# Performance work log

Measured on AMD Instinct MI355X. Metric: run time of the kernel, lower is better.

Reference implementation:

```python
import jax, jax.numpy as jnp
import numpy as np

B, T, D, S = 16, 16384, 256, 4
EPS = 1e-12  # matches torch F.normalize eps


def setup_inputs() -> dict:
    key = jax.random.key(0)
    k1, k2 = jax.random.split(key)
    embeddings = jax.random.normal(k1, (B, T, D), dtype=jnp.float32)
    spk = jax.random.randint(k2, (B, T), 0, S)
    labels = jax.nn.one_hot(spk, S, dtype=jnp.float32)  # [B,T,S] one-hot speaker indicators
    return {"embeddings": embeddings, "labels": labels}


def reference(embeddings, labels):
    # embeddings: [B,T,D], labels: [B,T,S]
    Bv, Tv, _ = embeddings.shape
    # row-wise L2 normalize (torch F.normalize semantics: v / max(||v||, eps))
    n = jnp.linalg.norm(embeddings, axis=-1, keepdims=True)
    V = embeddings / jnp.maximum(n, EPS)
    Y = labels
    # ||V V^T - Y Y^T||_F^2 = ||V^T V||_F^2 - 2||V^T Y||_F^2 + ||Y^T Y||_F^2
    Gvv = jnp.einsum('btd,bte->bde', V, V)   # [B,D,D]
    Gvy = jnp.einsum('btd,bts->bds', V, Y)   # [B,D,S]
    Gyy = jnp.einsum('bts,btu->bsu', Y, Y)   # [B,S,S]
    sq = lambda g: jnp.sum(g * g, axis=(1, 2))
    per_b = (sq(Gvv) - 2.0 * sq(Gvy) + sq(Gyy)) / (Tv * Tv)  # [B]
    return jnp.mean(per_b)
```

## Files before the change

### kernel.cpp

```cpp
#include <hip/hip_runtime.h>

#define NB 16
#define NT 16384
#define ND 256
#define NS 4
#define SLICES 16
#define TPB 1024
#define CHUNK 32
#define NITER (TPB / CHUNK)

typedef float          f32x4 __attribute__((ext_vector_type(4)));
typedef short          s16x8 __attribute__((ext_vector_type(8)));
typedef unsigned short u16x4 __attribute__((ext_vector_type(4)));

__device__ __forceinline__ unsigned short f2bf(float f) {
  unsigned int u = __float_as_uint(f);
  return (unsigned short)((u + 0x7FFFu + ((u >> 16) & 1u)) >> 16);
}

__global__ __launch_bounds__(512, 2) void fused_gram(
    const float* __restrict__ emb, const float* __restrict__ lab,
    float* __restrict__ Gvv, float* __restrict__ Gvy, float* __restrict__ Cnt)
{
  const int tid  = threadIdx.x;
  const int lane = tid & 63;
  const int w    = tid >> 6;
  const int b     = blockIdx.x >> 4;
  const int slice = blockIdx.x & 15;
  const int t0    = slice * TPB;

  __shared__ __align__(16) unsigned short rm[CHUNK * 260];
  __shared__ __align__(16) unsigned short blkT[4 * 256 * 8];
  __shared__ int   spk[TPB];
  __shared__ float cnt_lds[NS];

  if (tid < NS) cnt_lds[tid] = 0.0f;
  __syncthreads();

  {
    const f32x4* lv = (const f32x4*)(lab + ((size_t)b * NT + t0) * NS);
    for (int i = tid; i < TPB; i += 512) {
      f32x4 y = lv[i];
      int s = (int)(y.y + 2.0f * y.z + 3.0f * y.w + 0.5f);
      spk[i] = s;
      atomicAdd(&cnt_lds[s], 1.0f);
    }
  }

  const float* embB = emb + ((size_t)b * NT + t0) * ND;
  const int wr = w >> 2, wc = w & 3;

  f32x4 acc[8][4];
  #pragma unroll
  for (int i = 0; i < 8; ++i)
    #pragma unroll
    for (int j = 0; j < 4; ++j) acc[i][j] = (f32x4){0.f, 0.f, 0.f, 0.f};

  f32x4 pf[4];
  #pragma unroll
  for (int j = 0; j < 4; ++j)
    pf[j] = *(const f32x4*)(embB + (size_t)(w * 4 + j) * ND + 4 * lane);

  float rgvy0 = 0.f, rgvy1 = 0.f, rgvy2 = 0.f, rgvy3 = 0.f;

  for (int it = 0; it < NITER; ++it) {
    #pragma unroll
    for (int j = 0; j < 4; ++j) {
      f32x4 v = pf[j];
      float ss = v.x * v.x + v.y * v.y + v.z * v.z + v.w * v.w;
      #pragma unroll
      for (int off = 32; off; off >>= 1) ss += __shfl_xor(ss, off);
      float sc = 1.0f / fmaxf(sqrtf(ss), 1e-12f);
      u16x4 st;
      st.x = f2bf(v.x * sc); st.y = f2bf(v.y * sc);
      st.z = f2bf(v.z * sc); st.w = f2bf(v.w * sc);
      *(u16x4*)&rm[(w * 4 + j) * 260 + 4 * lane] = st;
    }
    if (it + 1 < NITER) {
      const float* p = embB + (size_t)((it + 1) * CHUNK + w * 4) * ND + 4 * lane;
      #pragma unroll
      for (int j = 0; j < 4; ++j) pf[j] = *(const f32x4*)(p + j * ND);
    }
    __syncthreads();

    #pragma unroll
    for (int pp = 0; pp < 2; ++pp) {
      int p  = tid + pp * 512;
      int tg = p >> 8, c = p & 255;
      int tb = tg * 8;
      s16x8 v8;
      #pragma unroll
      for (int s8 = 0; s8 < 8; ++s8) {
        unsigned short u = rm[(tb + s8) * 260 + c];
        v8[s8] = (short)u;
        float fv = __uint_as_float((unsigned int)u << 16);
        int sp = spk[it * CHUNK + tb + s8];
        rgvy0 += (sp == 0) ? fv : 0.0f;
        rgvy1 += (sp == 1) ? fv : 0.0f;
        rgvy2 += (sp == 2) ? fv : 0.0f;
        rgvy3 += (sp == 3) ? fv : 0.0f;
      }
      *(s16x8*)&blkT[p * 8] = v8;
    }
    __syncthreads();

    {
      const short* bp = (const short*)blkT;
      const int quad = lane >> 4, m16 = lane & 15;
      s16x8 afr[8];
      #pragma unroll
      for (int mi = 0; mi < 8; ++mi)
        afr[mi] = *(const s16x8*)(bp + (((quad << 8) + wr * 128 + mi * 16 + m16) << 3));
      #pragma unroll
      for (int mj = 0; mj < 4; ++mj) {
        s16x8 bfr = *(const s16x8*)(bp + (((quad << 8) + wc * 64 + mj * 16 + m16) << 3));
        #pragma unroll
        for (int mi = 0; mi < 8; ++mi)
          acc[mi][mj] = __builtin_amdgcn_mfma_f32_16x16x32_bf16(afr[mi], bfr, acc[mi][mj], 0, 0, 0);
      }
    }
  }

  {
    float* Gb = Gvv + (size_t)b * (ND * ND);
    const int quad = lane >> 4, m16 = lane & 15;
    #pragma unroll
    for (int mi = 0; mi < 8; ++mi)
      #pragma unroll
      for (int mj = 0; mj < 4; ++mj)
        #pragma unroll
        for (int r = 0; r < 4; ++r) {
          int row = wr * 128 + mi * 16 + quad * 4 + r;
          int col = wc * 64 + mj * 16 + m16;
          atomicAdd(&Gb[row * ND + col], acc[mi][mj][r]);
        }
  }
  {
    int c = tid & 255;
    float* gy = Gvy + (size_t)b * (NS * ND);
    atomicAdd(&gy[0 * ND + c], rgvy0);
    atomicAdd(&gy[1 * ND + c], rgvy1);
    atomicAdd(&gy[2 * ND + c], rgvy2);
    atomicAdd(&gy[3 * ND + c], rgvy3);
  }
  __syncthreads();
  if (tid < NS) atomicAdd(&Cnt[b * NS + tid], cnt_lds[tid]);
}

__global__ void finalize_kernel(const float* __restrict__ Gvv,
                                const float* __restrict__ Gvy,
                                const float* __restrict__ Cnt,
                                float* __restrict__ out)
{
  const int b = blockIdx.x >> 4, seg = blockIdx.x & 15;
  const int tid = threadIdx.x;
  float local = 0.f;
  const float* G = Gvv + (size_t)b * (ND * ND) + seg * 4096;
  for (int i = tid; i < 4096; i += 256) { float g = G[i]; local = fmaf(g, g, local); }
  if (seg == 0) {
    const float* gy = Gvy + (size_t)b * (NS * ND);
    for (int i = tid; i < NS * ND; i += 256) { float v = gy[i]; local = fmaf(-2.f * v, v, local); }
    if (tid < NS) { float c = Cnt[b * NS + tid]; local = fmaf(c, c, local); }
  }
  #pragma unroll
  for (int off = 32; off; off >>= 1) local += __shfl_xor(local, off);
  __shared__ float wsum[4];
  if ((tid & 63) == 0) wsum[tid >> 6] = local;
  __syncthreads();
  if (tid == 0) {
    float s = wsum[0] + wsum[1] + wsum[2] + wsum[3];
    atomicAdd(out, s * (1.0f / 4294967296.0f));
  }
}

extern "C" void kernel_launch(void* const* d_in, const int* in_sizes, int n_in,
                              void* d_out, int out_size, void* d_ws, size_t ws_size,
                              hipStream_t stream) {
  const float* emb = (const float*)d_in[0];
  const float* lab = (const float*)d_in[1];
  float* out = (float*)d_out;

  float* Gvv = (float*)d_ws;
  float* Gvy = Gvv + (size_t)NB * ND * ND;
  float* Cnt = Gvy + (size_t)NB * NS * ND;

  size_t zbytes = ((size_t)NB * ND * ND + (size_t)NB * NS * ND + NB * NS) * sizeof(float);
  hipMemsetAsync(d_ws, 0, zbytes, stream);
  hipMemsetAsync(d_out, 0, sizeof(float), stream);

  fused_gram<<<dim3(NB * SLICES), dim3(512), 0, stream>>>(emb, lab, Gvv, Gvy, Cnt);
  finalize_kernel<<<dim3(NB * SLICES), dim3(256), 0, stream>>>(Gvv, Gvy, Cnt, out);
}
```

Measured before the change: 418.8 us.

## Use 1024-thread blocks, MFMA for V^T Y, and per-slice partials instead of atomics

Blocks grow to 16 waves, each owning a 64x64 Gram tile with half the accumulators. V^T Y is now computed by an extra MFMA against a one-hot bf16 fragment built from 2-bit packed speaker ids, replacing the scalar per-element selects. Speaker counts come from wave ballots. The global atomicAdd reductions and the workspace memset are replaced by plain stores of per-slice partial Grams, which the finalize kernel sums. In exchange it writes and reads 64 MB of partials, removes LDS row padding (risking bank conflicts), and depends on a workspace large enough for the partials.

Result: slower. 474.3 us (+13.2%).

```diff
diff --git a/kernel.cpp b/kernel.cpp
--- a/kernel.cpp
+++ b/kernel.cpp
@@ -18,9 +18,9 @@
   return (unsigned short)((u + 0x7FFFu + ((u >> 16) & 1u)) >> 16);
 }
 
-__global__ __launch_bounds__(512, 2) void fused_gram(
+__global__ __launch_bounds__(1024) void fused_gram(
     const float* __restrict__ emb, const float* __restrict__ lab,
-    float* __restrict__ Gvv, float* __restrict__ Gvy, float* __restrict__ Cnt)
+    float* __restrict__ P, float* __restrict__ PY, float* __restrict__ CntP)
 {
   const int tid  = threadIdx.x;
   const int lane = tid & 63;
@@ -29,43 +29,53 @@
   const int slice = blockIdx.x & 15;
   const int t0    = slice * TPB;
 
-  __shared__ __align__(16) unsigned short rm[CHUNK * 260];
-  __shared__ __align__(16) unsigned short blkT[4 * 256 * 8];
-  __shared__ int   spk[TPB];
-  __shared__ float cnt_lds[NS];
-
-  if (tid < NS) cnt_lds[tid] = 0.0f;
+  __shared__ __align__(16) unsigned short rm[CHUNK * ND];
+  __shared__ __align__(16) unsigned short blkT[4 * ND * 8];
+  __shared__ unsigned int spk2[TPB / 16];
+  __shared__ float cnt_l[NS];
+
+  if (tid < TPB / 16) spk2[tid] = 0u;
+  if (tid < NS) cnt_l[tid] = 0.0f;
   __syncthreads();
 
   {
-    const f32x4* lv = (const f32x4*)(lab + ((size_t)b * NT + t0) * NS);
-    for (int i = tid; i < TPB; i += 512) {
-      f32x4 y = lv[i];
-      int s = (int)(y.y + 2.0f * y.z + 3.0f * y.w + 0.5f);
-      spk[i] = s;
-      atomicAdd(&cnt_lds[s], 1.0f);
+    f32x4 y = ((const f32x4*)(lab + ((size_t)b * NT + t0) * NS))[tid];
+    int s = (int)(y.y + 2.0f * y.z + 3.0f * y.w + 0.5f);
+    atomicOr(&spk2[tid >> 4], (unsigned)s << (2 * (tid & 15)));
+    unsigned long long m0 = __ballot(s == 0);
+    unsigned long long m1 = __ballot(s == 1);
+    unsigned long long m2 = __ballot(s == 2);
+    unsigned long long m3 = __ballot(s == 3);
+    if (lane == 0) {
+      atomicAdd(&cnt_l[0], (float)__popcll(m0));
+      atomicAdd(&cnt_l[1], (float)__popcll(m1));
+      atomicAdd(&cnt_l[2], (float)__popcll(m2));
+      atomicAdd(&cnt_l[3], (float)__popcll(m3));
     }
   }
 
   const float* embB = emb + ((size_t)b * NT + t0) * ND;
-  const int wr = w >> 2, wc = w & 3;
-
-  f32x4 acc[8][4];
+  const int r = w >> 2, c = w & 3;
+
+  f32x4 acc[4][4];
+  f32x4 yacc = (f32x4){0.f, 0.f, 0.f, 0.f};
   #pragma unroll
-  for (int i = 0; i < 8; ++i)
+  for (int i = 0; i < 4; ++i)
     #pragma unroll
     for (int j = 0; j < 4; ++j) acc[i][j] = (f32x4){0.f, 0.f, 0.f, 0.f};
 
-  f32x4 pf[4];
+  f32x4 pf[2];
   #pragma unroll
-  for (int j = 0; j < 4; ++j)
-    pf[j] = *(const f32x4*)(embB + (size_t)(w * 4 + j) * ND + 4 * lane);
-
-  float rgvy0 = 0.f, rgvy1 = 0.f, rgvy2 = 0.f, rgvy3 = 0.f;
+  for (int j = 0; j < 2; ++j)
+    pf[j] = *(const f32x4*)(embB + (size_t)(2 * w + j) * ND + 4 * lane);
+
+  __syncthreads();
+
+  const int quad = lane >> 4, m16 = lane & 15;
 
   for (int it = 0; it < NITER; ++it) {
     #pragma unroll
-    for (int j = 0; j < 4; ++j) {
+    for (int j = 0; j < 2; ++j) {
       f32x4 v = pf[j];
       float ss = v.x * v.x + v.y * v.y + v.z * v.z + v.w * v.w;
       #pragma unroll
@@ -74,93 +84,105 @@
       u16x4 st;
       st.x = f2bf(v.x * sc); st.y = f2bf(v.y * sc);
       st.z = f2bf(v.z * sc); st.w = f2bf(v.w * sc);
-      *(u16x4*)&rm[(w * 4 + j) * 260 + 4 * lane] = st;
+      *(u16x4*)&rm[(2 * w + j) * ND + 4 * lane] = st;
     }
     if (it + 1 < NITER) {
-      const float* p = embB + (size_t)((it + 1) * CHUNK + w * 4) * ND + 4 * lane;
-      #pragma unroll
-      for (int j = 0; j < 4; ++j) pf[j] = *(const f32x4*)(p + j * ND);
+      const float* p = embB + (size_t)((it + 1) * CHUNK + 2 * w) * ND + 4 * lane;
+      #pragma unroll
+      for (int j = 0; j < 2; ++j) pf[j] = *(const f32x4*)(p + j * ND);
     }
     __syncthreads();
 
-    #pragma unroll
-    for (int pp = 0; pp < 2; ++pp) {
-      int p  = tid + pp * 512;
-      int tg = p >> 8, c = p & 255;
-      int tb = tg * 8;
+    {
+      int tg = tid >> 8, d = tid & 255;
       s16x8 v8;
       #pragma unroll
-      for (int s8 = 0; s8 < 8; ++s8) {
-        unsigned short u = rm[(tb + s8) * 260 + c];
-        v8[s8] = (short)u;
-        float fv = __uint_as_float((unsigned int)u << 16);
-        int sp = spk[it * CHUNK + tb + s8];
-        rgvy0 += (sp == 0) ? fv : 0.0f;
-        rgvy1 += (sp == 1) ? fv : 0.0f;
-        rgvy2 += (sp == 2) ? fv : 0.0f;
-        rgvy3 += (sp == 3) ? fv : 0.0f;
-      }
-      *(s16x8*)&blkT[p * 8] = v8;
+      for (int s8 = 0; s8 < 8; ++s8)
+        v8[s8] = (short)rm[(tg * 8 + s8) * ND + d];
+      *(s16x8*)&blkT[(tg * ND + d) * 8] = v8;
     }
     __syncthreads();
 
     {
       const short* bp = (const short*)blkT;
-      const int quad = lane >> 4, m16 = lane & 15;
-      s16x8 afr[8];
-      #pragma unroll
-      for (int mi = 0; mi < 8; ++mi)
-        afr[mi] = *(const s16x8*)(bp + (((quad << 8) + wr * 128 + mi * 16 + m16) << 3));
-      #pragma unroll
-      for (int mj = 0; mj < 4; ++mj) {
-        s16x8 bfr = *(const s16x8*)(bp + (((quad << 8) + wc * 64 + mj * 16 + m16) << 3));
+      s16x8 afr[4];
+      #pragma unroll
+      for (int mi = 0; mi < 4; ++mi)
+        afr[mi] = *(const s16x8*)(bp + ((quad * ND + (4 * r + mi) * 16 + m16) << 3));
+
+      {
+        unsigned sw = spk2[it * 2 + (quad >> 1)];
+        s16x8 y8;
         #pragma unroll
-        for (int mi = 0; mi < 8; ++mi)
-          acc[mi][mj] = __builtin_amdgcn_mfma_f32_16x16x32_bf16(afr[mi], bfr, acc[mi][mj], 0, 0, 0);
+        for (int j = 0; j < 8; ++j) {
+          int sp = (int)((sw >> (2 * ((quad & 1) * 8 + j))) & 3u);
+          y8[j] = (sp == m16) ? (short)0x3F80 : (short)0;
+        }
+        yacc = __builtin_amdgcn_mfma_f32_16x16x32_bf16(afr[c], y8, yacc, 0, 0, 0);
       }
+
+      #pragma unroll
+      for (int nj = 0; nj < 4; ++nj) {
+        s16x8 bfr = *(const s16x8*)(bp + ((quad * ND + (4 * c + nj) * 16 + m16) << 3));
+        #pragma unroll
+        for (int mi = 0; mi < 4; ++mi)
+          acc[mi][nj] = __builtin_amdgcn_mfma_f32_16x16x32_bf16(afr[mi], bfr, acc[mi][nj], 0, 0, 0);
+      }
     }
   }
 
   {
-    float* Gb = Gvv + (size_t)b * (ND * ND);
-    const int quad = lane >> 4, m16 = lane & 15;
-    #pragma unroll
-    for (int mi = 0; mi < 8; ++mi)
-      #pragma unroll
-      for (int mj = 0; mj < 4; ++mj)
+    float* Pb = P + ((size_t)blockIdx.x << 16);
+    #pragma unroll
+    for (int mi = 0; mi < 4; ++mi)
+      #pragma unroll
+      for (int nj = 0; nj < 4; ++nj)
         #pragma unroll
-        for (int r = 0; r < 4; ++r) {
-          int row = wr * 128 + mi * 16 + quad * 4 + r;
-          int col = wc * 64 + mj * 16 + m16;
-          atomicAdd(&Gb[row * ND + col], acc[mi][mj][r]);
+        for (int rr = 0; rr < 4; ++rr) {
+          int row = r * 64 + mi * 16 + quad * 4 + rr;
+          int col = c * 64 + nj * 16 + m16;
+          Pb[row * ND + col] = acc[mi][nj][rr];
         }
-  }
-  {
-    int c = tid & 255;
-    float* gy = Gvy + (size_t)b * (NS * ND);
-    atomicAdd(&gy[0 * ND + c], rgvy0);
-    atomicAdd(&gy[1 * ND + c], rgvy1);
-    atomicAdd(&gy[2 * ND + c], rgvy2);
-    atomicAdd(&gy[3 * ND + c], rgvy3);
-  }
-  __syncthreads();
-  if (tid < NS) atomicAdd(&Cnt[b * NS + tid], cnt_lds[tid]);
-}
-
-__global__ void finalize_kernel(const float* __restrict__ Gvv,
-                                const float* __restrict__ Gvy,
-                                const float* __restrict__ Cnt,
-                                float* __restrict__ out)
+    float* PYb = PY + ((size_t)blockIdx.x << 12);
+    #pragma unroll
+    for (int rr = 0; rr < 4; ++rr)
+      PYb[(w * 16 + quad * 4 + rr) * 16 + m16] = yacc[rr];
+    if (tid < NS) CntP[blockIdx.x * NS + tid] = cnt_l[tid];
+  }
+}
+
+__global__ __launch_bounds__(256) void finalize_kernel(
+    const float* __restrict__ P, const float* __restrict__ PY,
+    const float* __restrict__ CntP, float* __restrict__ out)
 {
   const int b = blockIdx.x >> 4, seg = blockIdx.x & 15;
   const int tid = threadIdx.x;
   float local = 0.f;
-  const float* G = Gvv + (size_t)b * (ND * ND) + seg * 4096;
-  for (int i = tid; i < 4096; i += 256) { float g = G[i]; local = fmaf(g, g, local); }
+
+  const float* Pb = P + ((size_t)b * 16) * 65536 + seg * 4096;
+  #pragma unroll 4
+  for (int k = 0; k < 16; ++k) {
+    int e = tid + k * 256;
+    float g = 0.f;
+    #pragma unroll
+    for (int s = 0; s < 16; ++s) g += Pb[(size_t)s * 65536 + e];
+    local = fmaf(g, g, local);
+  }
   if (seg == 0) {
-    const float* gy = Gvy + (size_t)b * (NS * ND);
-    for (int i = tid; i < NS * ND; i += 256) { float v = gy[i]; local = fmaf(-2.f * v, v, local); }
-    if (tid < NS) { float c = Cnt[b * NS + tid]; local = fmaf(c, c, local); }
+    const float* Yb = PY + ((size_t)b * 16) * 4096;
+    #pragma unroll 4
+    for (int k = 0; k < 16; ++k) {
+      int e = tid + k * 256;
+      float g = 0.f;
+      #pragma unroll
+      for (int s = 0; s < 16; ++s) g += Yb[(size_t)s * 4096 + e];
+      local = fmaf(-2.f * g, g, local);
+    }
+    if (tid < NS) {
+      float ct = 0.f;
+      for (int s = 0; s < 16; ++s) ct += CntP[(b * 16 + s) * NS + tid];
+      local = fmaf(ct, ct, local);
+    }
   }
   #pragma unroll
   for (int off = 32; off; off >>= 1) local += __shfl_xor(local, off);
@@ -180,14 +202,12 @@
   const float* lab = (const float*)d_in[1];
   float* out = (float*)d_out;
 
-  float* Gvv = (float*)d_ws;
-  float* Gvy = Gvv + (size_t)NB * ND * ND;
-  float* Cnt = Gvy + (size_t)NB * NS * ND;
-
-  size_t zbytes = ((size_t)NB * ND * ND + (size_t)NB * NS * ND + NB * NS) * sizeof(float);
-  hipMemsetAsync(d_ws, 0, zbytes, stream);
+  float* P    = (float*)d_ws;
+  float* PY   = P + (size_t)256 * 65536;
+  float* CntP = PY + (size_t)256 * 4096;
+
   hipMemsetAsync(d_out, 0, sizeof(float), stream);
 
-  fused_gram<<<dim3(NB * SLICES), dim3(512), 0, stream>>>(emb, lab, Gvv, Gvy, Cnt);
-  finalize_kernel<<<dim3(NB * SLICES), dim3(256), 0, stream>>>(Gvv, Gvy, Cnt, out);
-}
+  fused_gram<<<dim3(NB * SLICES), dim3(1024), 0, stream>>>(emb, lab, P, PY, CntP);
+  finalize_kernel<<<dim3(NB * SLICES), dim3(256), 0, stream>>>(P, PY, CntP, out);
+}
```
